# Kernel tuning notes

Measured on AMD Instinct MI355X. Metric: run time of the kernel, lower is better.

The kernel has to match this reference:

```python
import jax, jax.numpy as jnp
import numpy as np
from jax import lax

B, H, W = 4096, 8, 8
DICT, SE, E, NZ = 64, 8, 256, 1024
C1, C2 = 64, 128
EPS = 1e-4


def setup_inputs() -> dict:
    key = jax.random.key(0)
    ks = jax.random.split(key, 32)
    d = {}
    d['s'] = jax.random.randint(ks[0], (B, H, W), 0, DICT)
    d['s_prime'] = jax.random.randint(ks[1], (B, H, W), 0, DICT)
    d['w_embed'] = jax.random.normal(ks[2], (DICT, SE), dtype=jnp.float32)
    i = 3
    for p in ('p1', 'p2', 'p3'):
        d[p + '_w1'] = jax.random.normal(ks[i], (C1, SE, 3, 3), dtype=jnp.float32) * 0.1; i += 1
        d[p + '_b1'] = jax.random.normal(ks[i], (C1,), dtype=jnp.float32) * 0.1; i += 1
        d[p + '_w2'] = jax.random.normal(ks[i], (C2, C1, 3, 3), dtype=jnp.float32) * 0.05; i += 1
        d[p + '_b2'] = jax.random.normal(ks[i], (C2,), dtype=jnp.float32) * 0.05; i += 1
        d[p + '_lw'] = jax.random.normal(ks[i], (E, C2 * H * W), dtype=jnp.float32) * 0.02; i += 1
        d[p + '_lb'] = jax.random.normal(ks[i], (E,), dtype=jnp.float32) * 0.02; i += 1
    d['z_vectors'] = jax.random.normal(ks[i], (NZ, E), dtype=jnp.float32)
    d['scale'] = jnp.ones((1,), dtype=jnp.float32)
    return d


def _conv(x, w, b):
    # x: [B,C,H,W], w: [O,I,3,3], padding=1 == SAME for k=3
    y = lax.conv_general_dilated(x, w, (1, 1), 'SAME',
                                 dimension_numbers=('NCHW', 'OIHW', 'NCHW'))
    return y + b[None, :, None, None]


def _phi(x, w1, b1, w2, b2, lw, lb):
    # run_modules(..., last_activation=True): relu after every conv
    x = jax.nn.relu(_conv(x, w1, b1))
    x = jax.nn.relu(_conv(x, w2, b2))
    x = x.reshape(x.shape[0], -1)  # [B, C2*H*W]
    return x @ lw.T + lb  # [B, E]


def _normalized(m, eps):
    return m / (jnp.sqrt(jnp.sum(m * m, axis=1, keepdims=True)) + eps)


def reference(s, s_prime, w_embed,
              p1_w1, p1_b1, p1_w2, p1_b2, p1_lw, p1_lb,
              p2_w1, p2_b1, p2_w2, p2_b2, p2_lw, p2_lb,
              p3_w1, p3_b1, p3_w2, p3_b2, p3_lw, p3_lb,
              z_vectors, scale):
    # nn.Embedding(max_norm=1): renorm rows with norm > 1 to unit norm
    wn = jnp.sqrt(jnp.sum(w_embed * w_embed, axis=1, keepdims=True))
    w = w_embed * jnp.minimum(1.0, 1.0 / jnp.maximum(wn, 1e-7))
    s_embed = jnp.transpose(w[s], (0, 3, 1, 2))        # [B,SE,H,W]
    sp_embed = jnp.transpose(w[s_prime], (0, 3, 1, 2))  # embed_conv is None -> identity

    s_int = _phi(s_embed, p1_w1, p1_b1, p1_w2, p1_b2, p1_lw, p1_lb)            # phi1
    diff_int = _phi(sp_embed - s_embed, p2_w1, p2_b1, p2_w2, p2_b2, p2_lw, p2_lb)  # phi2
    sp_out = _normalized(_phi(sp_embed, p3_w1, p3_b1, p3_w2, p3_b2, p3_lw, p3_lb), EPS)  # phi3

    # quantize: cdist (p=2) against codebook, argmax (farthest, as in source), gather
    x2 = jnp.sum(diff_int * diff_int, axis=1, keepdims=True)      # [B,1]
    z2 = jnp.sum(z_vectors * z_vectors, axis=1)[None, :]          # [1,NZ]
    dist = jnp.sqrt(jnp.maximum(x2 + z2 - 2.0 * (diff_int @ z_vectors.T), 0.0))  # [B,NZ]
    z_inds = jnp.argmax(dist, axis=1)                              # [B]
    z_matrix = z_vectors[z_inds]                                   # [B,E]

    s_out = _normalized(s_int + z_matrix, EPS)                     # fc (fc_sizes=None)
    gram = s_out @ sp_out.T                                        # [B,B]
    return jnp.exp(scale) * gram
```

## Files before the change

kernel.cpp:

```cpp
#include <hip/hip_runtime.h>
#include <hip/hip_bf16.h>
#include <math.h>

#define NB 4096
#define SE 8
#define ND 64
#define C1 64
#define C2 128
#define NE 256
#define NZ 1024
#define CHUNK 2048
#define KACT 8192
#define KSPLIT 8

#define W1M_N (3*64*96)
#define W2M_N (3*128*576)
#define ZT_N  (256*1024)
#define PREP_TOTAL (W1M_N + W2M_N + ZT_N)
#define LW_N (NE*KACT)

typedef __attribute__((ext_vector_type(8))) short bf16x8;
typedef __attribute__((ext_vector_type(4))) float f32x4;
typedef __attribute__((ext_vector_type(8))) unsigned short u16x8;
typedef __attribute__((ext_vector_type(4))) unsigned short u16x4;

static __device__ __forceinline__ unsigned short f2bf(float v) {
  __hip_bfloat16 h = __float2bfloat16(v);
  return __builtin_bit_cast(unsigned short, h);
}
static __device__ __forceinline__ float bf2f(unsigned short u) {
  return __bfloat162float(__builtin_bit_cast(__hip_bfloat16, u));
}

__global__ __launch_bounds__(256) void prep_kernel(
    const float* __restrict__ w1_0, const float* __restrict__ w1_1, const float* __restrict__ w1_2,
    const float* __restrict__ w2_0, const float* __restrict__ w2_1, const float* __restrict__ w2_2,
    const float* __restrict__ z,
    unsigned short* __restrict__ w1mh, unsigned short* __restrict__ w1ml,
    unsigned short* __restrict__ w2mh, unsigned short* __restrict__ w2ml,
    float* __restrict__ zT)
{
  int idx = blockIdx.x * 256 + threadIdx.x;
  if (idx < W1M_N) {
    int p = idx / 6144; int r = idx - p*6144; int o = r / 96; int q = r - o*96;
    int j = q >> 3; int c = q & 7;
    const float* w1 = (p == 0) ? w1_0 : (p == 1) ? w1_1 : w1_2;
    float v = (j < 9) ? w1[o*72 + c*9 + j] : 0.f;
    unsigned short h = f2bf(v);
    w1mh[idx] = h;
    w1ml[idx] = f2bf(v - bf2f(h));
  } else if (idx < W1M_N + W2M_N) {
    int r0 = idx - W1M_N;
    int p = r0 / (128*576); int r = r0 - p*(128*576);
    int o = r / 576; int rem = r - o*576; int j = rem >> 6; int c = rem & 63;
    const float* w2 = (p == 0) ? w2_0 : (p == 1) ? w2_1 : w2_2;
    float v = w2[o*576 + c*9 + j];
    unsigned short h = f2bf(v);
    w2mh[r0] = h;
    w2ml[r0] = f2bf(v - bf2f(h));
  } else if (idx < PREP_TOTAL) {
    int r = idx - (W1M_N + W2M_N);
    int e = r >> 10, n = r & 1023;
    zT[r] = z[n*256 + e];
  }
}

__global__ __launch_bounds__(256) void prep_lw_kernel(
    const float* __restrict__ lw, unsigned short* __restrict__ lwh,
    unsigned short* __restrict__ lwl, int do_lo)
{
  int idx = blockIdx.x * 256 + threadIdx.x;
  float v = lw[idx];
  unsigned short h = f2bf(v);
  lwh[idx] = h;
  if (do_lo) lwl[idx] = f2bf(v - bf2f(h));
}

template<int PASSES>
__global__ __launch_bounds__(256, 4) void conv_phi_kernel(
    const int* __restrict__ s, const int* __restrict__ sp,
    const float* __restrict__ w_embed,
    const unsigned short* __restrict__ w1mh, const unsigned short* __restrict__ w1ml,
    const float* __restrict__ b1,
    const unsigned short* __restrict__ w2mh, const unsigned short* __restrict__ w2ml,
    const float* __restrict__ b2,
    unsigned short* __restrict__ acth, unsigned short* __restrict__ actl,
    int mode, int b_start)
{
  __shared__ float wtab[ND][SE];
  __shared__ int sidx[64];
  __shared__ int spidx[64];
  __shared__ __align__(16) unsigned short xph[960];
  __shared__ __align__(16) unsigned short xpl[960];
  __shared__ __align__(16) unsigned short c1h[7680];
  __shared__ __align__(16) unsigned short c1l[7680];

  const int tid = threadIdx.x;
  const int b = b_start + blockIdx.x;

  {
    int4 z4 = {0,0,0,0};
    for (int t = tid; t < 120; t += 256) { ((int4*)xph)[t] = z4; ((int4*)xpl)[t] = z4; }
    for (int t = tid; t < 960; t += 256) { ((int4*)c1h)[t] = z4; ((int4*)c1l)[t] = z4; }
  }

  if (tid < 64) {
    sidx[tid] = s[b*64 + tid];
    float v[SE]; float ss = 0.f;
    #pragma unroll
    for (int c = 0; c < SE; ++c) { v[c] = w_embed[tid*SE + c]; ss += v[c]*v[c]; }
    float nrm = sqrtf(ss);
    float sc = fminf(1.f, 1.f / fmaxf(nrm, 1e-7f));
    #pragma unroll
    for (int c = 0; c < SE; ++c) wtab[tid][c] = v[c] * sc;
  } else if (tid < 128) {
    spidx[tid - 64] = sp[b*64 + tid - 64];
  }
  __syncthreads();

  if (tid < 64) {
    const int y = tid >> 3, x = tid & 7;
    const float* r0 = wtab[sidx[tid]];
    const float* r1 = wtab[spidx[tid]];
    u16x8 hv, lv;
    #pragma unroll
    for (int c = 0; c < SE; ++c) {
      float e0 = r0[c], e1 = r1[c];
      float v = (mode == 0) ? e0 : (mode == 1) ? (e1 - e0) : e1;
      unsigned short h = f2bf(v);
      hv[c] = h;
      lv[c] = f2bf(v - bf2f(h));
    }
    const int lin = (y + 1)*12 + (x + 1);
    *(u16x8*)(xph + lin*8) = hv;
    *(u16x8*)(xpl + lin*8) = lv;
  }
  __syncthreads();

  {
    const int lane = tid & 63, wid = tid >> 6;
    const int ph = wid;
    const int l15 = lane & 15, lk4 = lane >> 4;

    f32x4 a1[4];
    #pragma unroll
    for (int fm = 0; fm < 4; ++fm) a1[fm] = (f32x4){0.f,0.f,0.f,0.f};

    #pragma unroll
    for (int kk = 0; kk < 3; ++kk) {
      const int j = (kk << 2) + lk4;
      const int jc = (j > 8) ? 8 : j;
      const int dy = jc / 3, dx = jc - 3*(jc/3);
      bf16x8 Wh[4], Wl[4];
      #pragma unroll
      for (int fm = 0; fm < 4; ++fm) {
        const int o = (fm << 4) + l15;
        Wh[fm] = *(const bf16x8*)(w1mh + o*96 + (kk << 5) + (lk4 << 3));
        Wl[fm] = *(const bf16x8*)(w1ml + o*96 + (kk << 5) + (lk4 << 3));
      }
      const int p = (ph << 4) + l15;
      const int lin = ((p >> 3) + dy)*12 + (p & 7) + dx;
      const bf16x8 Xh = *(const bf16x8*)(xph + (lin << 3));
      const bf16x8 Xl = *(const bf16x8*)(xpl + (lin << 3));
      __builtin_amdgcn_s_setprio(1);
      #pragma unroll
      for (int fm = 0; fm < 4; ++fm) {
        a1[fm] = __builtin_amdgcn_mfma_f32_16x16x32_bf16(Wh[fm], Xh, a1[fm], 0, 0, 0);
        a1[fm] = __builtin_amdgcn_mfma_f32_16x16x32_bf16(Wl[fm], Xh, a1[fm], 0, 0, 0);
        a1[fm] = __builtin_amdgcn_mfma_f32_16x16x32_bf16(Wh[fm], Xl, a1[fm], 0, 0, 0);
      }
      __builtin_amdgcn_s_setprio(0);
    }

    const int p = (ph << 4) + l15;
    const int lin = ((p >> 3) + 1)*12 + (p & 7) + 1;
    #pragma unroll
    for (int fm = 0; fm < 4; ++fm) {
      const int obase = (fm << 4) + (lk4 << 2);
      const float4 bv = *(const float4*)(b1 + obase);
      const int cb = obase >> 3;
      const int osub = obase & 7;
      const int idx2 = (lin << 6) + ((cb ^ (lin & 7)) << 3) + osub;
      u16x4 hv, lv;
      {
        float v0 = fmaxf(a1[fm][0] + bv.x, 0.f);
        float v1 = fmaxf(a1[fm][1] + bv.y, 0.f);
        float v2 = fmaxf(a1[fm][2] + bv.z, 0.f);
        float v3 = fmaxf(a1[fm][3] + bv.w, 0.f);
        hv[0] = f2bf(v0); hv[1] = f2bf(v1); hv[2] = f2bf(v2); hv[3] = f2bf(v3);
        lv[0] = f2bf(v0 - bf2f(hv[0])); lv[1] = f2bf(v1 - bf2f(hv[1]));
        lv[2] = f2bf(v2 - bf2f(hv[2])); lv[3] = f2bf(v3 - bf2f(hv[3]));
      }
      *(u16x4*)(c1h + idx2) = hv;
      *(u16x4*)(c1l + idx2) = lv;
    }
  }
  __syncthreads();

  {
    const int lane = tid & 63, wid = tid >> 6;
    const int ob = wid << 5;
    const int l15 = lane & 15, lk4 = lane >> 4;
    const int y0b = l15 >> 3, x0 = l15 & 7;

    f32x4 acc[4][2];
    #pragma unroll
    for (int mf = 0; mf < 4; ++mf)
      #pragma unroll
      for (int nf = 0; nf < 2; ++nf) acc[mf][nf] = (f32x4){0.f,0.f,0.f,0.f};

    #pragma unroll
    for (int j = 0; j < 9; ++j) {
      const int dy = j / 3, dx = j - 3*(j/3);
      #pragma unroll
      for (int h2 = 0; h2 < 2; ++h2) {
        const int kofs = j*64 + h2*32 + lk4*8;
        bf16x8 Bh[2], Bl[2];
        #pragma unroll
        for (int nf = 0; nf < 2; ++nf) {
          const int orow = ob + (nf << 4) + l15;
          Bh[nf] = *(const bf16x8*)(w2mh + orow*576 + kofs);
          if (PASSES == 3) Bl[nf] = *(const bf16x8*)(w2ml + orow*576 + kofs);
        }
        const int cbk = (h2 << 2) + lk4;
        bf16x8 Ah[4], Al[4];
        #pragma unroll
        for (int mf = 0; mf < 4; ++mf) {
          const int lin = ((mf << 1) + y0b + dy)*12 + x0 + dx;
          const int idx2 = (lin << 6) + ((cbk ^ (lin & 7)) << 3);
          Ah[mf] = *(const bf16x8*)(c1h + idx2);
          Al[mf] = *(const bf16x8*)(c1l + idx2);
        }
        __builtin_amdgcn_s_setprio(1);
        #pragma unroll
        for (int mf = 0; mf < 4; ++mf) {
          #pragma unroll
          for (int nf = 0; nf < 2; ++nf) {
            acc[mf][nf] = __builtin_amdgcn_mfma_f32_16x16x32_bf16(Ah[mf], Bh[nf], acc[mf][nf], 0, 0, 0);
            acc[mf][nf] = __builtin_amdgcn_mfma_f32_16x16x32_bf16(Al[mf], Bh[nf], acc[mf][nf], 0, 0, 0);
            if (PASSES == 3)
              acc[mf][nf] = __builtin_amdgcn_mfma_f32_16x16x32_bf16(Ah[mf], Bl[nf], acc[mf][nf], 0, 0, 0);
          }
        }
        __builtin_amdgcn_s_setprio(0);
      }
    }

    const size_t rowbase = (size_t)blockIdx.x * 8192;
    #pragma unroll
    for (int nf = 0; nf < 2; ++nf) {
      const int col = ob + (nf << 4) + l15;
      const float bv = b2[col];
      #pragma unroll
      for (int mf = 0; mf < 4; ++mf) {
        const int p0 = mf*16 + lk4*4;
        u16x4 hv, lv;
        #pragma unroll
        for (int r2 = 0; r2 < 4; ++r2) {
          float v = fmaxf(acc[mf][nf][r2] + bv, 0.f);
          unsigned short hq = f2bf(v);
          hv[r2] = hq;
          lv[r2] = f2bf(v - bf2f(hq));
        }
        *(u16x4*)(acth + rowbase + col*64 + p0) = hv;
        if (PASSES == 3)
          *(u16x4*)(actl + rowbase + col*64 + p0) = lv;
      }
    }
  }
}

template<int PASSES>
__global__ __launch_bounds__(256) void gemm_lds_tn(
    const unsigned short* __restrict__ Ahp, const unsigned short* __restrict__ Alp,
    const unsigned short* __restrict__ Bhp, const unsigned short* __restrict__ Blp,
    int K, float* __restrict__ Cdirect, float* __restrict__ Cpart,
    const float* __restrict__ bias, const float* __restrict__ scale_ptr)
{
  constexpr int NOP = (PASSES == 3) ? 2 : 1;
  __shared__ __align__(16) unsigned short As[NOP][128*64];
  __shared__ __align__(16) unsigned short Bs[NOP][64*64];

  const int tid = threadIdx.x;
  const int lane = tid & 63, wid = tid >> 6;
  const int wm = wid >> 1, wn = wid & 1;
  const int l15 = lane & 15, lk4 = lane >> 4;
  const int M = gridDim.x << 7, N = gridDim.y << 6;
  const int KC = K / gridDim.z;
  const int bm = blockIdx.x << 7, bn = blockIdx.y << 6;
  const int kbase = blockIdx.z * KC;
  const int NT = KC >> 6;

  const int sr = tid >> 3;
  const int sc8 = (tid & 7) * 8;

  const unsigned short* gA[NOP];
  const unsigned short* gB[NOP];
  gA[0] = Ahp; gB[0] = Bhp;
  if (PASSES == 3) { gA[1] = Alp; gB[1] = Blp; }

  u16x8 ra[NOP][4], rb[NOP][2];

  f32x4 acc[4][2];
  #pragma unroll
  for (int fm = 0; fm < 4; ++fm)
    #pragma unroll
    for (int nf = 0; nf < 2; ++nf) acc[fm][nf] = (f32x4){0.f,0.f,0.f,0.f};

  {
    const int k0 = kbase + sc8;
    #pragma unroll
    for (int p = 0; p < NOP; ++p) {
      #pragma unroll
      for (int i = 0; i < 4; ++i)
        ra[p][i] = *(const u16x8*)(gA[p] + (size_t)(bm + sr + i*32) * K + k0);
      #pragma unroll
      for (int i = 0; i < 2; ++i)
        rb[p][i] = *(const u16x8*)(gB[p] + (size_t)(bn + sr + i*32) * K + k0);
    }
  }

  for (int t = 0; t < NT; ++t) {
    __syncthreads();
    #pragma unroll
    for (int p = 0; p < NOP; ++p) {
      #pragma unroll
      for (int i = 0; i < 4; ++i) {
        const int r = sr + i*32;
        *(u16x8*)(&As[p][r*64 + (sc8 ^ ((r & 7) << 3))]) = ra[p][i];
      }
      #pragma unroll
      for (int i = 0; i < 2; ++i) {
        const int r = sr + i*32;
        *(u16x8*)(&Bs[p][r*64 + (sc8 ^ ((r & 7) << 3))]) = rb[p][i];
      }
    }
    __syncthreads();
    if (t + 1 < NT) {
      const int k0 = kbase + ((t + 1) << 6) + sc8;
      #pragma unroll
      for (int p = 0; p < NOP; ++p) {
        #pragma unroll
        for (int i = 0; i < 4; ++i)
          ra[p][i] = *(const u16x8*)(gA[p] + (size_t)(bm + sr + i*32) * K + k0);
        #pragma unroll
        for (int i = 0; i < 2; ++i)
          rb[p][i] = *(const u16x8*)(gB[p] + (size_t)(bn + sr + i*32) * K + k0);
      }
    }
    #pragma unroll
    for (int ks = 0; ks < 2; ++ks) {
      const int kb = ks*32 + lk4*8;
      bf16x8 af[NOP][4], bf[NOP][2];
      #pragma unroll
      for (int p = 0; p < NOP; ++p) {
        #pragma unroll
        for (int fm = 0; fm < 4; ++fm) {
          const int r = wm*64 + fm*16 + l15;
          af[p][fm] = *(const bf16x8*)(&As[p][r*64 + (kb ^ ((r & 7) << 3))]);
        }
        #pragma unroll
        for (int nf = 0; nf < 2; ++nf) {
          const int r = wn*32 + nf*16 + l15;
          bf[p][nf] = *(const bf16x8*)(&Bs[p][r*64 + (kb ^ ((r & 7) << 3))]);
        }
      }
      #pragma unroll
      for (int fm = 0; fm < 4; ++fm) {
        #pragma unroll
        for (int nf = 0; nf < 2; ++nf) {
          acc[fm][nf] = __builtin_amdgcn_mfma_f32_16x16x32_bf16(af[0][fm], bf[0][nf], acc[fm][nf], 0, 0, 0);
          if (PASSES == 3) {
            acc[fm][nf] = __builtin_amdgcn_mfma_f32_16x16x32_bf16(af[0][fm], bf[1][nf], acc[fm][nf], 0, 0, 0);
            acc[fm][nf] = __builtin_amdgcn_mfma_f32_16x16x32_bf16(af[1][fm], bf[0][nf], acc[fm][nf], 0, 0, 0);
          }
        }
      }
    }
  }

  if (Cpart) {
    float* base = Cpart + (size_t)blockIdx.z * ((size_t)M * N);
    #pragma unroll
    for (int fm = 0; fm < 4; ++fm) {
      #pragma unroll
      for (int nf = 0; nf < 2; ++nf) {
        const int row0 = bm + wm*64 + fm*16 + lk4*4;
        const int col  = bn + wn*32 + nf*16 + l15;
        #pragma unroll
        for (int r2 = 0; r2 < 4; ++r2)
          base[(size_t)(row0 + r2) * N + col] = acc[fm][nf][r2];
      }
    }
  } else {
    float alpha = scale_ptr ? expf(scale_ptr[0]) : 1.f;
    #pragma unroll
    for (int fm = 0; fm < 4; ++fm) {
      #pragma unroll
      for (int nf = 0; nf < 2; ++nf) {
        const int row0 = bm + wm*64 + fm*16 + lk4*4;
        const int col  = bn + wn*32 + nf*16 + l15;
        const float bv = bias ? bias[col] : 0.f;
        #pragma unroll
        for (int r2 = 0; r2 < 4; ++r2)
          Cdirect[(size_t)(row0 + r2) * N + col] = alpha * acc[fm][nf][r2] + bv;
      }
    }
  }
}

__global__ __launch_bounds__(256) void reduce_bias_kernel(
    const float* __restrict__ part, const float* __restrict__ bias, float* __restrict__ out)
{
  const int idx = blockIdx.x * 256 + threadIdx.x;
  float a = bias[idx & (NE-1)];
  #pragma unroll
  for (int q = 0; q < KSPLIT; ++q) a += part[(size_t)q * (CHUNK*NE) + idx];
  out[idx] = a;
}

__global__ __launch_bounds__(256) void quant_kernel(
    const float* __restrict__ diff, const float* __restrict__ zT, int* __restrict__ z_ind)
{
  __shared__ __align__(16) float d[8][NE];
  __shared__ float wv[8][4];
  __shared__ int wni[8][4];
  const int tid = threadIdx.x;
  const int b0 = blockIdx.x * 8;
  for (int j = tid; j < 8*NE; j += 256) (&d[0][0])[j] = diff[(size_t)b0*NE + j];
  __syncthreads();

  float zz[4] = {0.f, 0.f, 0.f, 0.f};
  float dot[8][4] = {};
  for (int e = 0; e < NE; e += 4) {
    float4 dd[8];
    #pragma unroll
    for (int r = 0; r < 8; ++r) dd[r] = *(const float4*)(&d[r][e]);
    #pragma unroll
    for (int u = 0; u < 4; ++u) {
      const float* zr = zT + (size_t)(e + u) * NZ + tid;
      float z0 = zr[0], z1 = zr[256], z2 = zr[512], z3 = zr[768];
      zz[0] = fmaf(z0, z0, zz[0]); zz[1] = fmaf(z1, z1, zz[1]);
      zz[2] = fmaf(z2, z2, zz[2]); zz[3] = fmaf(z3, z3, zz[3]);
      #pragma unroll
      for (int r = 0; r < 8; ++r) {
        const float de = (u == 0) ? dd[r].x : (u == 1) ? dd[r].y : (u == 2) ? dd[r].z : dd[r].w;
        dot[r][0] = fmaf(z0, de, dot[r][0]);
        dot[r][1] = fmaf(z1, de, dot[r][1]);
        dot[r][2] = fmaf(z2, de, dot[r][2]);
        dot[r][3] = fmaf(z3, de, dot[r][3]);
      }
    }
  }

  const int lane = tid & 63, wid = tid >> 6;
  #pragma unroll
  for (int r = 0; r < 8; ++r) {
    float best = zz[0] - 2.f*dot[r][0]; int bi = tid;
    float v1 = zz[1] - 2.f*dot[r][1]; if (v1 > best) { best = v1; bi = tid + 256; }
    float v2 = zz[2] - 2.f*dot[r][2]; if (v2 > best) { best = v2; bi = tid + 512; }
    float v3 = zz[3] - 2.f*dot[r][3]; if (v3 > best) { best = v3; bi = tid + 768; }
    for (int m = 1; m < 64; m <<= 1) {
      float ov = __shfl_xor(best, m, 64);
      int   oi = __shfl_xor(bi, m, 64);
      if (ov > best || (ov == best && oi < bi)) { best = ov; bi = oi; }
    }
    if (lane == 0) { wv[r][wid] = best; wni[r][wid] = bi; }
  }
  __syncthreads();
  if (tid < 8) {
    float best = wv[tid][0]; int bi = wni[tid][0];
    #pragma unroll
    for (int w = 1; w < 4; ++w) {
      float v = wv[tid][w]; int n = wni[tid][w];
      if (v > best || (v == best && n < bi)) { best = v; bi = n; }
    }
    z_ind[b0 + tid] = bi;
  }
}

__global__ __launch_bounds__(256) void norm_to_bf16_kernel(
    const float* __restrict__ v, unsigned short* __restrict__ ob)
{
  const int row = blockIdx.x*4 + (threadIdx.x >> 6);
  const int lane = threadIdx.x & 63;
  float4 x = ((const float4*)v)[(size_t)row*64 + lane];
  float ss = x.x*x.x + x.y*x.y + x.z*x.z + x.w*x.w;
  #pragma unroll
  for (int m = 1; m < 64; m <<= 1) ss += __shfl_xor(ss, m, 64);
  float sc = 1.f / (sqrtf(ss) + 1e-4f);
  u16x4 o;
  o[0] = f2bf(x.x*sc); o[1] = f2bf(x.y*sc); o[2] = f2bf(x.z*sc); o[3] = f2bf(x.w*sc);
  *(u16x4*)(ob + (size_t)row*NE + lane*4) = o;
}

__global__ __launch_bounds__(256) void build_sout_kernel(
    const float* __restrict__ s_int, const float* __restrict__ z,
    const int* __restrict__ z_ind, unsigned short* __restrict__ ob)
{
  const int row = blockIdx.x*4 + (threadIdx.x >> 6);
  const int lane = threadIdx.x & 63;
  const int zi = z_ind[row];
  float4 a = *((const float4*)s_int + (size_t)row*64 + lane);
  float4 c = *((const float4*)z + (size_t)zi*64 + lane);
  float4 x = {a.x + c.x, a.y + c.y, a.z + c.z, a.w + c.w};
  float ss = x.x*x.x + x.y*x.y + x.z*x.z + x.w*x.w;
  #pragma unroll
  for (int m = 1; m < 64; m <<= 1) ss += __shfl_xor(ss, m, 64);
  float sc = 1.f / (sqrtf(ss) + 1e-4f);
  u16x4 o;
  o[0] = f2bf(x.x*sc); o[1] = f2bf(x.y*sc); o[2] = f2bf(x.z*sc); o[3] = f2bf(x.w*sc);
  *(u16x4*)(ob + (size_t)row*NE + lane*4) = o;
}

extern "C" void kernel_launch(void* const* d_in, const int* in_sizes, int n_in,
                              void* d_out, int out_size, void* d_ws, size_t ws_size,
                              hipStream_t stream)
{
  const int* s  = (const int*)d_in[0];
  const int* sp = (const int*)d_in[1];
  const float* w_embed = (const float*)d_in[2];
  const float* z = (const float*)d_in[21];
  const float* scale = (const float*)d_in[22];
  float* out = (float*)d_out;

  size_t off = 0;
  auto allocB = [&](size_t bytes) -> void* {
    void* p = (void*)((char*)d_ws + off);
    off += ((bytes + 255) & ~(size_t)255);
    return p;
  };
  unsigned short* w1mh  = (unsigned short*)allocB((size_t)W1M_N * 2);
  unsigned short* w1ml  = (unsigned short*)allocB((size_t)W1M_N * 2);
  unsigned short* w2mh  = (unsigned short*)allocB((size_t)W2M_N * 2);
  unsigned short* w2ml  = (unsigned short*)allocB((size_t)W2M_N * 2);
  float* zT             = (float*)allocB(ZT_N * 4);
  unsigned short* lwh   = (unsigned short*)allocB((size_t)LW_N * 2);
  unsigned short* lwl   = (unsigned short*)allocB((size_t)LW_N * 2);
  float* s_int          = (float*)allocB((size_t)NB * NE * 4);
  float* diff_int       = (float*)allocB((size_t)NB * NE * 4);
  float* sp_out         = (float*)allocB((size_t)NB * NE * 4);
  unsigned short* soutb = (unsigned short*)allocB((size_t)NB * NE * 2);
  unsigned short* spoutb= (unsigned short*)allocB((size_t)NB * NE * 2);
  int*   z_ind          = (int*)allocB(NB * 4);
  float* part           = (float*)allocB((size_t)CHUNK * NE * KSPLIT * 4);

  unsigned short* acth = (unsigned short*)d_out;
  unsigned short* actl = acth + (size_t)CHUNK * KACT;

  prep_kernel<<<PREP_TOTAL/256, 256, 0, stream>>>(
      (const float*)d_in[3],  (const float*)d_in[9],  (const float*)d_in[15],
      (const float*)d_in[5],  (const float*)d_in[11], (const float*)d_in[17],
      z, w1mh, w1ml, w2mh, w2ml, zT);

  for (int phi = 0; phi < 3; ++phi) {
    const float* b1 = (const float*)d_in[4 + phi*6];
    const float* b2 = (const float*)d_in[6 + phi*6];
    const float* lw = (const float*)d_in[7 + phi*6];
    const float* lb = (const float*)d_in[8 + phi*6];
    float* outvec = (phi == 0) ? s_int : (phi == 1) ? diff_int : sp_out;

    prep_lw_kernel<<<LW_N/256, 256, 0, stream>>>(lw, lwh, lwl, phi == 1);

    for (int b0 = 0; b0 < NB; b0 += CHUNK) {
      if (phi == 1)
        conv_phi_kernel<3><<<CHUNK, 256, 0, stream>>>(
            s, sp, w_embed, w1mh + phi*6144, w1ml + phi*6144, b1,
            w2mh + phi*(128*576), w2ml + phi*(128*576), b2,
            acth, actl, phi, b0);
      else
        conv_phi_kernel<2><<<CHUNK, 256, 0, stream>>>(
            s, sp, w_embed, w1mh + phi*6144, w1ml + phi*6144, b1,
            w2mh + phi*(128*576), w2ml + phi*(128*576), b2,
            acth, actl, phi, b0);
      dim3 g(CHUNK/128, NE/64, KSPLIT);
      if (phi == 1)
        gemm_lds_tn<3><<<g, 256, 0, stream>>>(acth, actl, lwh, lwl,
            KACT, nullptr, part, nullptr, nullptr);
      else
        gemm_lds_tn<1><<<g, 256, 0, stream>>>(acth, nullptr, lwh, nullptr,
            KACT, nullptr, part, nullptr, nullptr);
      reduce_bias_kernel<<<(CHUNK*NE)/256, 256, 0, stream>>>(part, lb, outvec + (size_t)b0*NE);
    }
  }

  norm_to_bf16_kernel<<<NB/4, 256, 0, stream>>>(sp_out, spoutb);
  quant_kernel<<<NB/8, 256, 0, stream>>>(diff_int, zT, z_ind);
  build_sout_kernel<<<NB/4, 256, 0, stream>>>(s_int, z, z_ind, soutb);

  dim3 gg(NB/128, NB/64, 1);
  gemm_lds_tn<1><<<gg, 256, 0, stream>>>(soutb, nullptr, spoutb, nullptr,
      NE, out, nullptr, nullptr, scale);
}
```

Measured before the change: 656.0 us.

## Double-buffer conv2 operand loads and switch c1 LDS layout to channel-block planes

```diff
diff --git a/kernel.cpp b/kernel.cpp
--- a/kernel.cpp
+++ b/kernel.cpp
@@ -178,9 +178,7 @@
     for (int fm = 0; fm < 4; ++fm) {
       const int obase = (fm << 4) + (lk4 << 2);
       const float4 bv = *(const float4*)(b1 + obase);
-      const int cb = obase >> 3;
-      const int osub = obase & 7;
-      const int idx2 = (lin << 6) + ((cb ^ (lin & 7)) << 3) + osub;
+      const int idx2 = (obase >> 3)*960 + lin*8 + (obase & 7);
       u16x4 hv, lv;
       {
         float v0 = fmaxf(a1[fm][0] + bv.x, 0.f);
@@ -202,6 +200,7 @@
     const int ob = wid << 5;
     const int l15 = lane & 15, lk4 = lane >> 4;
     const int y0b = l15 >> 3, x0 = l15 & 7;
+    constexpr int PFA = (PASSES == 2);
 
     f32x4 acc[4][2];
     #pragma unroll
@@ -209,42 +208,60 @@
       #pragma unroll
       for (int nf = 0; nf < 2; ++nf) acc[mf][nf] = (f32x4){0.f,0.f,0.f,0.f};
 
-    #pragma unroll
-    for (int j = 0; j < 9; ++j) {
-      const int dy = j / 3, dx = j - 3*(j/3);
-      #pragma unroll
-      for (int h2 = 0; h2 < 2; ++h2) {
-        const int kofs = j*64 + h2*32 + lk4*8;
-        bf16x8 Bh[2], Bl[2];
+    bf16x8 Bh[2][2], Bl[2][2];
+    bf16x8 Ah[2][4], Al[2][4];
+
+    #define LOADB(t, buf)                                                        \
+      {                                                                          \
+        const int j_ = (t) >> 1, h2_ = (t) & 1;                                  \
+        const int kofs_ = j_*64 + h2_*32 + lk4*8;                                \
+        _Pragma("unroll")                                                        \
+        for (int nf = 0; nf < 2; ++nf) {                                         \
+          const int orow_ = ob + (nf << 4) + l15;                                \
+          Bh[buf][nf] = *(const bf16x8*)(w2mh + orow_*576 + kofs_);              \
+          if (PASSES == 3) Bl[buf][nf] = *(const bf16x8*)(w2ml + orow_*576 + kofs_); \
+        }                                                                        \
+      }
+    #define LOADA(t, buf)                                                        \
+      {                                                                          \
+        const int j_ = (t) >> 1, h2_ = (t) & 1;                                  \
+        const int dy_ = j_ / 3, dx_ = j_ - 3*(j_/3);                             \
+        const int cbk_ = (h2_ << 2) + lk4;                                       \
+        _Pragma("unroll")                                                        \
+        for (int mf = 0; mf < 4; ++mf) {                                         \
+          const int lin_ = ((mf << 1) + y0b + dy_)*12 + x0 + dx_;                \
+          const int a_ = cbk_*960 + lin_*8;                                      \
+          Ah[buf][mf] = *(const bf16x8*)(c1h + a_);                              \
+          Al[buf][mf] = *(const bf16x8*)(c1l + a_);                              \
+        }                                                                        \
+      }
+
+    LOADB(0, 0);
+    if (PFA) LOADA(0, 0);
+
+    #pragma unroll
+    for (int t = 0; t < 18; ++t) {
+      const int cur = t & 1, nxt = cur ^ 1;
+      if (t < 17) {
+        LOADB(t + 1, nxt);
+        if (PFA) LOADA(t + 1, nxt);
+      }
+      if (!PFA) LOADA(t, cur);
+      __builtin_amdgcn_s_setprio(1);
+      #pragma unroll
+      for (int mf = 0; mf < 4; ++mf) {
         #pragma unroll
         for (int nf = 0; nf < 2; ++nf) {
-          const int orow = ob + (nf << 4) + l15;
-          Bh[nf] = *(const bf16x8*)(w2mh + orow*576 + kofs);
-          if (PASSES == 3) Bl[nf] = *(const bf16x8*)(w2ml + orow*576 + kofs);
+          acc[mf][nf] = __builtin_amdgcn_mfma_f32_16x16x32_bf16(Ah[cur][mf], Bh[cur][nf], acc[mf][nf], 0, 0, 0);
+          acc[mf][nf] = __builtin_amdgcn_mfma_f32_16x16x32_bf16(Al[cur][mf], Bh[cur][nf], acc[mf][nf], 0, 0, 0);
+          if (PASSES == 3)
+            acc[mf][nf] = __builtin_amdgcn_mfma_f32_16x16x32_bf16(Ah[cur][mf], Bl[cur][nf], acc[mf][nf], 0, 0, 0);
         }
-        const int cbk = (h2 << 2) + lk4;
-        bf16x8 Ah[4], Al[4];
-        #pragma unroll
-        for (int mf = 0; mf < 4; ++mf) {
-          const int lin = ((mf << 1) + y0b + dy)*12 + x0 + dx;
-          const int idx2 = (lin << 6) + ((cbk ^ (lin & 7)) << 3);
-          Ah[mf] = *(const bf16x8*)(c1h + idx2);
-          Al[mf] = *(const bf16x8*)(c1l + idx2);
-        }
-        __builtin_amdgcn_s_setprio(1);
-        #pragma unroll
-        for (int mf = 0; mf < 4; ++mf) {
-          #pragma unroll
-          for (int nf = 0; nf < 2; ++nf) {
-            acc[mf][nf] = __builtin_amdgcn_mfma_f32_16x16x32_bf16(Ah[mf], Bh[nf], acc[mf][nf], 0, 0, 0);
-            acc[mf][nf] = __builtin_amdgcn_mfma_f32_16x16x32_bf16(Al[mf], Bh[nf], acc[mf][nf], 0, 0, 0);
-            if (PASSES == 3)
-              acc[mf][nf] = __builtin_amdgcn_mfma_f32_16x16x32_bf16(Ah[mf], Bl[nf], acc[mf][nf], 0, 0, 0);
-          }
-        }
-        __builtin_amdgcn_s_setprio(0);
-      }
-    }
+      }
+      __builtin_amdgcn_s_setprio(0);
+    }
+    #undef LOADB
+    #undef LOADA
 
     const size_t rowbase = (size_t)blockIdx.x * 8192;
     #pragma unroll
```

New measurement: 689.1 us. 5.0% more time.

## Re-layout conv weights tap-major and conv1 activations channel-block-major

Applied to the files above, without the earlier changes.

```diff
diff --git a/kernel.cpp b/kernel.cpp
--- a/kernel.cpp
+++ b/kernel.cpp
@@ -13,8 +13,8 @@
 #define KACT 8192
 #define KSPLIT 8
 
-#define W1M_N (3*64*96)
-#define W2M_N (3*128*576)
+#define W1M_N (3*12*64*8)
+#define W2M_N (3*18*128*32)
 #define ZT_N  (256*1024)
 #define PREP_TOTAL (W1M_N + W2M_N + ZT_N)
 #define LW_N (NE*KACT)
@@ -42,8 +42,8 @@
 {
   int idx = blockIdx.x * 256 + threadIdx.x;
   if (idx < W1M_N) {
-    int p = idx / 6144; int r = idx - p*6144; int o = r / 96; int q = r - o*96;
-    int j = q >> 3; int c = q & 7;
+    int p = idx / 6144; int r = idx - p*6144;
+    int j = r >> 9; int rem = r & 511; int o = rem >> 3; int c = rem & 7;
     const float* w1 = (p == 0) ? w1_0 : (p == 1) ? w1_1 : w1_2;
     float v = (j < 9) ? w1[o*72 + c*9 + j] : 0.f;
     unsigned short h = f2bf(v);
@@ -56,8 +56,9 @@
     const float* w2 = (p == 0) ? w2_0 : (p == 1) ? w2_1 : w2_2;
     float v = w2[o*576 + c*9 + j];
     unsigned short h = f2bf(v);
-    w2mh[r0] = h;
-    w2ml[r0] = f2bf(v - bf2f(h));
+    const int d = p*(128*576) + ((j << 1) + (c >> 5))*4096 + o*32 + (c & 31);
+    w2mh[d] = h;
+    w2ml[d] = f2bf(v - bf2f(h));
   } else if (idx < PREP_TOTAL) {
     int r = idx - (W1M_N + W2M_N);
     int e = r >> 10, n = r & 1023;
@@ -87,7 +88,7 @@
     unsigned short* __restrict__ acth, unsigned short* __restrict__ actl,
     int mode, int b_start)
 {
-  __shared__ float wtab[ND][SE];
+  __shared__ float wtab[ND][SE+1];
   __shared__ int sidx[64];
   __shared__ int spidx[64];
   __shared__ __align__(16) unsigned short xph[960];
@@ -155,8 +156,8 @@
       #pragma unroll
       for (int fm = 0; fm < 4; ++fm) {
         const int o = (fm << 4) + l15;
-        Wh[fm] = *(const bf16x8*)(w1mh + o*96 + (kk << 5) + (lk4 << 3));
-        Wl[fm] = *(const bf16x8*)(w1ml + o*96 + (kk << 5) + (lk4 << 3));
+        Wh[fm] = *(const bf16x8*)(w1mh + (j << 9) + (o << 3));
+        Wl[fm] = *(const bf16x8*)(w1ml + (j << 9) + (o << 3));
       }
       const int p = (ph << 4) + l15;
       const int lin = ((p >> 3) + dy)*12 + (p & 7) + dx;
@@ -178,9 +179,7 @@
     for (int fm = 0; fm < 4; ++fm) {
       const int obase = (fm << 4) + (lk4 << 2);
       const float4 bv = *(const float4*)(b1 + obase);
-      const int cb = obase >> 3;
-      const int osub = obase & 7;
-      const int idx2 = (lin << 6) + ((cb ^ (lin & 7)) << 3) + osub;
+      const int idx2 = (obase >> 3)*960 + lin*8 + (obase & 7);
       u16x4 hv, lv;
       {
         float v0 = fmaxf(a1[fm][0] + bv.x, 0.f);
@@ -214,22 +213,23 @@
       const int dy = j / 3, dx = j - 3*(j/3);
       #pragma unroll
       for (int h2 = 0; h2 < 2; ++h2) {
-        const int kofs = j*64 + h2*32 + lk4*8;
+        const int sbase = ((j << 1) + h2) << 12;
         bf16x8 Bh[2], Bl[2];
         #pragma unroll
         for (int nf = 0; nf < 2; ++nf) {
           const int orow = ob + (nf << 4) + l15;
-          Bh[nf] = *(const bf16x8*)(w2mh + orow*576 + kofs);
-          if (PASSES == 3) Bl[nf] = *(const bf16x8*)(w2ml + orow*576 + kofs);
+          const int a = sbase + orow*32 + (lk4 << 3);
+          Bh[nf] = *(const bf16x8*)(w2mh + a);
+          if (PASSES == 3) Bl[nf] = *(const bf16x8*)(w2ml + a);
         }
         const int cbk = (h2 << 2) + lk4;
         bf16x8 Ah[4], Al[4];
         #pragma unroll
         for (int mf = 0; mf < 4; ++mf) {
           const int lin = ((mf << 1) + y0b + dy)*12 + x0 + dx;
-          const int idx2 = (lin << 6) + ((cbk ^ (lin & 7)) << 3);
-          Ah[mf] = *(const bf16x8*)(c1h + idx2);
-          Al[mf] = *(const bf16x8*)(c1l + idx2);
+          const int a = cbk*960 + lin*8;
+          Ah[mf] = *(const bf16x8*)(c1h + a);
+          Al[mf] = *(const bf16x8*)(c1l + a);
         }
         __builtin_amdgcn_s_setprio(1);
         #pragma unroll
```

Result: faster. 531.4 us (-19.0%).
